# Kernel tuning notes

Hardware: AMD Instinct MI355X
Metric: run time of the kernel (lower is better)

The kernel has to match this reference:

```python
import jax, jax.numpy as jnp
import numpy as np
from jax import lax

B, H, W = 256, 60, 180
NB, NH, OUTC = 37, 128, 64
FILTERS = [1, 64, 128, 128, 64]
FEAT_H, FEAT_W = 4, 12  # spatial dims after 4 SAME 2x2 maxpools
D_LSTM = FEAT_H * OUTC  # 256
LEAK = 0.01
EPS = 1e-5


def setup_inputs() -> dict:
    key = jax.random.key(0)
    ks = jax.random.split(key, 32)
    inp = {"x": jax.random.normal(ks[0], (B, H, W, 1), dtype=jnp.float32)}
    for i in range(4):
        cin, cout = FILTERS[i], FILTERS[i + 1]
        inp[f"w{i}"] = jax.random.normal(ks[1 + i], (3, 3, cin, cout), dtype=jnp.float32) / np.sqrt(9.0 * cin)
        inp[f"cb{i}"] = jnp.zeros((cout,), jnp.float32)
        inp[f"g{i}"] = jnp.ones((cout,), jnp.float32)
        inp[f"bb{i}"] = jnp.zeros((cout,), jnp.float32)
        inp[f"mm{i}"] = 0.1 * jax.random.normal(ks[5 + i], (cout,), dtype=jnp.float32)
        inp[f"mv{i}"] = jax.random.uniform(ks[9 + i], (cout,), minval=0.5, maxval=1.5, dtype=jnp.float32)
    inp["lW0"] = jax.random.normal(ks[13], (D_LSTM + NH, 4 * NH), dtype=jnp.float32) / np.sqrt(D_LSTM + NH)
    inp["lb0"] = jnp.zeros((4 * NH,), jnp.float32)
    inp["lW1"] = jax.random.normal(ks[14], (NH + NH, 4 * NH), dtype=jnp.float32) / np.sqrt(2 * NH)
    inp["lb1"] = jnp.zeros((4 * NH,), jnp.float32)
    inp["Wout"] = jax.random.normal(ks[15], (NH, NB), dtype=jnp.float32) / np.sqrt(NH)
    inp["bout"] = jnp.zeros((NB,), jnp.float32)
    return inp


def _conv_block(x, w, cb, g, bb, mm, mv):
    x = lax.conv_general_dilated(x, w, (1, 1), 'SAME',
                                 dimension_numbers=('NHWC', 'HWIO', 'NHWC')) + cb
    x = (x - mm) * (g * lax.rsqrt(mv + EPS)) + bb          # inference batch norm
    x = jnp.where(x < 0, LEAK * x, x)                       # leaky relu
    x = lax.reduce_window(x, -jnp.inf, lax.max, (1, 2, 2, 1), (1, 2, 2, 1), 'SAME')
    return x


def _lstm_step(c, h, xt, Wk, bk):
    # TF LSTMCell: gates [i, j, f, o], forget_bias=1.0
    z = jnp.concatenate([xt, h], axis=-1) @ Wk + bk
    i, j, f, o = jnp.split(z, 4, axis=-1)
    c = c * jax.nn.sigmoid(f + 1.0) + jax.nn.sigmoid(i) * jnp.tanh(j)
    h = jnp.tanh(c) * jax.nn.sigmoid(o)
    return c, h


def reference(x, w0, cb0, g0, bb0, mm0, mv0, w1, cb1, g1, bb1, mm1, mv1,
              w2, cb2, g2, bb2, mm2, mv2, w3, cb3, g3, bb3, mm3, mv3,
              lW0, lb0, lW1, lb1, Wout, bout):
    for w, cb, g, bb, mm, mv in [(w0, cb0, g0, bb0, mm0, mv0),
                                 (w1, cb1, g1, bb1, mm1, mv1),
                                 (w2, cb2, g2, bb2, mm2, mv2),
                                 (w3, cb3, g3, bb3, mm3, mv3)]:
        x = _conv_block(x, w, cb, g, bb, mm, mv)
    # x: [B, 4, 12, 64] -> [B, T=12, 256]
    x = jnp.transpose(x, (0, 2, 1, 3)).reshape(x.shape[0], FEAT_W, FEAT_H * OUTC)
    xs = jnp.transpose(x, (1, 0, 2))  # [T, B, D]
    b = x.shape[0]
    zeros = jnp.zeros((b, NH), x.dtype)

    def step(carry, xt):
        c0, h0, c1, h1 = carry
        c0, h0 = _lstm_step(c0, h0, xt, lW0, lb0)
        c1, h1 = _lstm_step(c1, h1, h0, lW1, lb1)
        return (c0, h0, c1, h1), h1

    _, hs = lax.scan(step, (zeros, zeros, zeros, zeros), xs)  # [T, B, NH]
    logits = hs @ Wout + bout  # [T, B, nb_classes] (time-major, as in the TF graph)
    return logits
```

## Files before the change

### kernel.cpp

```cpp
#include <hip/hip_runtime.h>
#include <hip/hip_bf16.h>
#include <math.h>
#include <stdint.h>

#define EPS 1e-5f
#define LEAK 0.01f
#define NEG_INF (-3.402823e38f)

typedef __attribute__((ext_vector_type(8))) short short8v;
typedef __attribute__((ext_vector_type(4))) float f32x4;

__device__ __forceinline__ float sigm(float x){ return 1.0f/(1.0f + __expf(-x)); }
__device__ __forceinline__ float tanhf_(float x){ return 1.0f - 2.0f/(__expf(2.0f*x)+1.0f); }
__device__ __forceinline__ float bnl(float a, float sc, float sh){
    float v = fmaf(a, sc, sh);
    return v < 0.0f ? LEAK*v : v;
}
__device__ __forceinline__ unsigned short f2bf(float f){
    __hip_bfloat16 h = __float2bfloat16(f);
    return *reinterpret_cast<unsigned short*>(&h);
}
__device__ __forceinline__ float bf2f(unsigned short u){
    return __uint_as_float(((unsigned)u) << 16);
}

__global__ __launch_bounds__(256) void setup_k(
    const float* __restrict__ w1, const float* __restrict__ w2, const float* __restrict__ w3,
    const float* __restrict__ lW0, const float* __restrict__ lW1, const float* __restrict__ Wout,
    const float* __restrict__ cb0, const float* __restrict__ g0, const float* __restrict__ bb0,
    const float* __restrict__ mm0, const float* __restrict__ mv0,
    const float* __restrict__ cb1, const float* __restrict__ g1, const float* __restrict__ bb1,
    const float* __restrict__ mm1, const float* __restrict__ mv1,
    const float* __restrict__ cb2, const float* __restrict__ g2, const float* __restrict__ bb2,
    const float* __restrict__ mm2, const float* __restrict__ mv2,
    const float* __restrict__ cb3, const float* __restrict__ g3, const float* __restrict__ bb3,
    const float* __restrict__ mm3, const float* __restrict__ mv3,
    unsigned short* __restrict__ Wp1, unsigned short* __restrict__ Wp2, unsigned short* __restrict__ Wp3,
    unsigned short* __restrict__ Wx0p, unsigned short* __restrict__ Wh0p,
    unsigned short* __restrict__ Wx1p, unsigned short* __restrict__ Wh1p,
    unsigned short* __restrict__ WoT, float* __restrict__ bns)
{
    const int bid = blockIdx.x, tid = threadIdx.x;
    if (bid < 864){
        const float* w; unsigned short* wp; int CIN, COUT, base;
        if (bid < 288){ w = w1; wp = Wp1; CIN=64; COUT=128; base = bid; }
        else { w = w2; wp = Wp2; CIN=128; COUT=128; base = bid-288; }
        int t = base*256 + tid;
        int total = 9*CIN*COUT;
        if (t < total){
            int cout = t % COUT, k = t / COUT;
            wp[(size_t)(k>>3)*COUT*8 + (size_t)cout*8 + (k&7)] = f2bf(w[(size_t)k*COUT + cout]);
        }
        return;
    }
    if (bid < 1152){
        int t = (bid-864)*256 + tid;
        if (t < 73728){
            int cout = t % 64, k = t / 64;
            Wp3[(size_t)(k>>3)*64*8 + (size_t)cout*8 + (k&7)] = f2bf(w3[(size_t)k*64 + cout]);
        }
        return;
    }
    if (bid < 2432){
        const float* src; unsigned short* dst; int base;
        if (bid < 1664){ src = lW0; dst = Wx0p; base = bid-1152; }
        else if (bid < 1920){ src = lW0 + 256*512; dst = Wh0p; base = bid-1664; }
        else if (bid < 2176){ src = lW1; dst = Wx1p; base = bid-1920; }
        else { src = lW1 + 128*512; dst = Wh1p; base = bid-2176; }
        int t = base*256 + tid;
        int k = t >> 9, col = t & 511;
        dst[(size_t)(k>>3)*4096 + col*8 + (k&7)] = f2bf(src[(size_t)k*512 + col]);
        return;
    }
    if (bid < 2451){
        int t = (bid-2432)*256 + tid;
        if (t < 4736){
            int n = t >> 7, k = t & 127;
            WoT[t] = f2bf(Wout[k*37 + n]);
        }
        return;
    }
    {
        int t = (bid-2451)*256 + tid;
        if (t < 128){
            float s = g1[t]*rsqrtf(mv1[t]+EPS);
            bns[t] = s; bns[128+t] = fmaf(cb1[t]-mm1[t], s, bb1[t]);
        } else if (t < 256){
            int u = t-128;
            float s = g2[u]*rsqrtf(mv2[u]+EPS);
            bns[256+u] = s; bns[384+u] = fmaf(cb2[u]-mm2[u], s, bb2[u]);
        } else if (t < 320){
            int u = t-256;
            float s = g3[u]*rsqrtf(mv3[u]+EPS);
            bns[512+u] = s; bns[576+u] = fmaf(cb3[u]-mm3[u], s, bb3[u]);
        } else if (t < 384){
            int u = t-320;
            float s = g0[u]*rsqrtf(mv0[u]+EPS);
            bns[640+u] = s; bns[704+u] = fmaf(cb0[u]-mm0[u], s, bb0[u]);
        }
        return;
    }
}

__global__ __launch_bounds__(256) void conv0_k(
    const float* __restrict__ x, const float* __restrict__ w,
    const float* __restrict__ bsc, const float* __restrict__ bsh,
    unsigned short* __restrict__ out, int bbase, int total)
{
    __shared__ float wv[576];
    __shared__ float scs[64], shs[64];
    const int tid = threadIdx.x;
    for (int i=tid;i<576;i+=256) wv[i] = w[i];
    if (tid < 64){ scs[tid]=bsc[tid]; shs[tid]=bsh[tid]; }
    __syncthreads();
    const int id = blockIdx.x*256 + tid;
    if (id >= total) return;
    const int px = id % 90; int r = id / 90; const int py = r % 30; const int b0 = r / 30;
    const float* xb = x + (size_t)(bbase+b0)*10800;
    float p[4][4];
    const int y0 = 2*py-1, xx0 = 2*px-1;
#pragma unroll
    for (int rr=0;rr<4;rr++){
        int yy=y0+rr;
#pragma unroll
        for (int cc=0;cc<4;cc++){
            int xc=xx0+cc;
            p[rr][cc] = (yy>=0&&yy<60&&xc>=0&&xc<180)? xb[yy*180+xc] : 0.f;
        }
    }
    unsigned short* ob = out + (size_t)id*64;
#pragma unroll
    for (int cg=0;cg<8;cg++){
        short8v o8;
#pragma unroll
        for (int j=0;j<8;j++){
            const int co = cg*8+j;
            float s00=0.f,s01=0.f,s10=0.f,s11=0.f;
#pragma unroll
            for (int ky=0;ky<3;ky++)
#pragma unroll
            for (int kx=0;kx<3;kx++){
                float wt = wv[(ky*3+kx)*64+co];
                s00 = fmaf(p[ky][kx],     wt, s00);
                s01 = fmaf(p[ky][kx+1],   wt, s01);
                s10 = fmaf(p[ky+1][kx],   wt, s10);
                s11 = fmaf(p[ky+1][kx+1], wt, s11);
            }
            float sc=scs[co], sh=shs[co];
            float m = fmaxf(fmaxf(bnl(s00,sc,sh),bnl(s01,sc,sh)),
                            fmaxf(bnl(s10,sc,sh),bnl(s11,sc,sh)));
            o8[j] = (short)f2bf(m);
        }
        *(short8v*)&ob[cg*8] = o8;
    }
}

template<int CIN,int COUT,int H,int W>
__global__ __launch_bounds__(256,4) void convmf_k(
    const unsigned short* __restrict__ in, const unsigned short* __restrict__ wp,
    const float* __restrict__ bsc, const float* __restrict__ bsh,
    unsigned short* __restrict__ out)
{
    constexpr int PH=(H+1)/2, PW=(W+1)/2;
    constexpr int HALVES = CIN/64;
    constexpr int NIT = 9*HALVES;
    constexpr int NREP = COUT/16;
    constexpr int CH = (64*COUT)/(256*8);
    __shared__ alignas(16) unsigned short wls[3][64*COUT];

    const int tid = threadIdx.x;
    const int lane = tid & 63;
    const int wm = tid >> 6;
    const int l15 = lane & 15, l4 = lane >> 4;
    const int x0 = blockIdx.x*16, y0 = blockIdx.y*8;
    const int b = blockIdx.z;
    const unsigned short* inb = in + (size_t)b*H*W*CIN;

    int rowoff[4]; bool rowok[4];
#pragma unroll
    for (int j=0;j<4;j++){
        int gy = y0 + 2*wm - 1 + j;
        rowok[j] = (unsigned)gy < (unsigned)H;
        rowoff[j] = (rowok[j] ? gy : 0) * (W*CIN);
    }
    int coloff[3]; bool colok[3];
#pragma unroll
    for (int kx=0;kx<3;kx++){
        int gx = x0 + l15 + kx - 1;
        colok[kx] = (unsigned)gx < (unsigned)W;
        coloff[kx] = (colok[kx] ? gx : 0) * CIN;
    }

    f32x4 acc[2][NREP];
#pragma unroll
    for (int m=0;m<2;m++)
#pragma unroll
    for (int n=0;n<NREP;n++) acc[m][n] = f32x4{0.f,0.f,0.f,0.f};

    auto stageB = [&](int it, int buf){
        const unsigned short* src = wp + (size_t)(it*8)*(COUT*8);
#pragma unroll
        for (int i=0;i<CH;i++){
            const unsigned short* g = src + (size_t)(tid + i*256)*8;
            unsigned short* l = &wls[buf][((tid & ~63) + i*256)*8];
            __builtin_amdgcn_global_load_lds(
                (const __attribute__((address_space(1))) unsigned int*)(uintptr_t)g,
                (__attribute__((address_space(3))) unsigned int*)(uintptr_t)l,
                16, 0, 0);
        }
    };

    stageB(0, 0);
    if (NIT > 1) stageB(1, 1);
    if constexpr (CH == 4){ asm volatile("s_waitcnt vmcnt(4)" ::: "memory"); }
    else                  { asm volatile("s_waitcnt vmcnt(2)" ::: "memory"); }
    __builtin_amdgcn_sched_barrier(0);
    __builtin_amdgcn_s_barrier();

    for (int it=0; it<NIT; ++it){
        const int tap = it / HALVES;
        const int khalf = it - tap*HALVES;
        const int ky = tap/3, kx = tap - ky*3;
        const int cin0 = khalf*64 + l4*8;
        const short8v z8 = short8v{0,0,0,0,0,0,0,0};
        short8v a[2][2];
#pragma unroll
        for (int rf=0;rf<2;rf++){
            const int j = rf + ky;
            const bool ok = rowok[j] && colok[kx];
            const unsigned short* p = inb + rowoff[j] + coloff[kx] + cin0;
#pragma unroll
            for (int ks=0;ks<2;ks++){
                short8v v = *(const short8v*)(p + ks*32);
                a[rf][ks] = ok ? v : z8;
            }
        }
        __builtin_amdgcn_sched_barrier(0);
        if (it+2 < NIT) stageB(it+2, (it+2)%3);
        __builtin_amdgcn_sched_barrier(0);
        const unsigned short* wb = &wls[it%3][0];
        __builtin_amdgcn_s_setprio(1);
#pragma unroll
        for (int ks=0; ks<2; ++ks){
#pragma unroll
            for (int nf=0; nf<NREP; ++nf){
                short8v bfr = *(const short8v*)&wb[((ks*4+l4)*COUT + nf*16 + l15)*8];
                acc[0][nf] = __builtin_amdgcn_mfma_f32_16x16x32_bf16(a[0][ks], bfr, acc[0][nf],0,0,0);
                acc[1][nf] = __builtin_amdgcn_mfma_f32_16x16x32_bf16(a[1][ks], bfr, acc[1][nf],0,0,0);
            }
        }
        __builtin_amdgcn_s_setprio(0);
        __builtin_amdgcn_s_barrier();
    }

    const int pr = (y0>>1) + wm;
    if (pr < PH){
        const bool r1 = (y0 + 2*wm + 1) < H;
        unsigned short* ob = out + ((size_t)b*PH + pr)*PW*COUT;
#pragma unroll
        for (int nf=0; nf<NREP; ++nf){
            const int co = nf*16 + l15;
            const float scv = bsc[co], shv = bsh[co];
            f32x4 e = acc[0][nf], o = acc[1][nf];
#pragma unroll
            for (int pp=0; pp<2; ++pp){
                const int pc = (x0>>1) + l4*2 + pp;
                if (pc >= PW) continue;
                const int oddcol = x0 + l4*4 + 2*pp + 1;
                float m = bnl(e[2*pp], scv, shv);
                if (oddcol < W) m = fmaxf(m, bnl(e[2*pp+1], scv, shv));
                if (r1){
                    m = fmaxf(m, bnl(o[2*pp], scv, shv));
                    if (oddcol < W) m = fmaxf(m, bnl(o[2*pp+1], scv, shv));
                }
                ob[(size_t)pc*COUT + co] = f2bf(m);
            }
        }
    }
}

template<int K, int MODE>
__global__ __launch_bounds__(256) void gemmrow_k(
    const unsigned short* __restrict__ A, const unsigned short* __restrict__ wp,
    const float* __restrict__ bias, float* __restrict__ out)
{
    constexpr int NS = K/32;
    __shared__ alignas(16) unsigned short wls[2][16384];
    const int tid = threadIdx.x, lane = tid & 63, w = tid >> 6;
    const int l15 = lane & 15, l4 = lane >> 4;
    const int r0 = blockIdx.x*32;

    f32x4 acc[2][8];
#pragma unroll
    for (int m=0;m<2;m++)
#pragma unroll
    for (int n=0;n<8;n++) acc[m][n] = f32x4{0.f,0.f,0.f,0.f};

    auto stage = [&](int s, int buf){
        const unsigned short* src = wp + (size_t)s*16384;
#pragma unroll
        for (int i=0;i<8;i++){
            int e = (tid + i*256)*8;
            *(short8v*)&wls[buf][e] = *(const short8v*)&src[e];
        }
    };
    stage(0,0);
    __syncthreads();

    for (int s=0;s<NS;++s){
        const int k0 = s*32 + l4*8;
        short8v af[2];
#pragma unroll
        for (int mf=0;mf<2;++mf){
            const int row = r0 + mf*16 + l15;
            size_t idx;
            if constexpr (MODE == 0){
                const int b = row & 255, t = row >> 8;
                idx = (size_t)b*3072 + (k0>>6)*768 + t*64 + (k0&63);
            } else {
                idx = (size_t)row*K + k0;
            }
            af[mf] = *(const short8v*)&A[idx];
        }
        if (s+1 < NS) stage(s+1,(s+1)&1);
        const unsigned short* wb = &wls[s&1][0];
#pragma unroll
        for (int nf=0;nf<8;++nf){
            const int col = w*128 + nf*16 + l15;
            short8v bfr = *(const short8v*)&wb[(l4*512 + col)*8];
#pragma unroll
            for (int mf=0;mf<2;++mf)
                acc[mf][nf] = __builtin_amdgcn_mfma_f32_16x16x32_bf16(af[mf], bfr, acc[mf][nf], 0,0,0);
        }
        __syncthreads();
    }
#pragma unroll
    for (int nf=0;nf<8;++nf){
        const int col = w*128 + nf*16 + l15;
        const float bv = bias[col];
#pragma unroll
        for (int mf=0;mf<2;++mf){
#pragma unroll
            for (int j=0;j<4;++j){
                const int row = r0 + mf*16 + l4*4 + j;
                out[(size_t)row*512 + col] = acc[mf][nf][j] + bv;
            }
        }
    }
}

__global__ __launch_bounds__(512) void lstm0_k(
    const float* __restrict__ xp, const unsigned short* __restrict__ wh0p,
    unsigned short* __restrict__ h0g)
{
    __shared__ alignas(16) unsigned short wl[65536];
    __shared__ alignas(16) float hb[128];
    __shared__ float zs[512];
    const int col = threadIdx.x;
    const int b = blockIdx.x;
#pragma unroll
    for (int i=0;i<16;i++){
        int e = (col + i*512)*8;
        *(short8v*)&wl[e] = *(const short8v*)&wh0p[e];
    }
    if (col < 128) hb[col] = 0.f;
    float c0 = 0.f;
    __syncthreads();

    for (int t=0;t<12;t++){
        float acc = xp[((size_t)t*256 + b)*512 + col];
#pragma unroll 4
        for (int kg=0;kg<16;kg++){
            short8v w8 = *(const short8v*)&wl[(kg*512 + col)*8];
            float4 hlo = *(const float4*)&hb[kg*8];
            float4 hhi = *(const float4*)&hb[kg*8+4];
            acc = fmaf(bf2f((unsigned short)w8[0]), hlo.x, acc);
            acc = fmaf(bf2f((unsigned short)w8[1]), hlo.y, acc);
            acc = fmaf(bf2f((unsigned short)w8[2]), hlo.z, acc);
            acc = fmaf(bf2f((unsigned short)w8[3]), hlo.w, acc);
            acc = fmaf(bf2f((unsigned short)w8[4]), hhi.x, acc);
            acc = fmaf(bf2f((unsigned short)w8[5]), hhi.y, acc);
            acc = fmaf(bf2f((unsigned short)w8[6]), hhi.z, acc);
            acc = fmaf(bf2f((unsigned short)w8[7]), hhi.w, acc);
        }
        zs[col] = acc;
        __syncthreads();
        if (col < 128){
            float zi=zs[col], zj=zs[128+col], zf=zs[256+col], zo=zs[384+col];
            c0 = c0*sigm(zf+1.f) + sigm(zi)*tanhf_(zj);
            float h = tanhf_(c0)*sigm(zo);
            hb[col] = h;
            h0g[((size_t)t*256 + b)*128 + col] = f2bf(h);
        }
        __syncthreads();
    }
}

__global__ __launch_bounds__(512) void lstm1_k(
    const float* __restrict__ zp1, const unsigned short* __restrict__ wh1p,
    const unsigned short* __restrict__ woT, const float* __restrict__ bout,
    float* __restrict__ out)
{
    __shared__ alignas(16) unsigned short wl[65536];
    __shared__ alignas(16) float hb[128];
    __shared__ float zs[512];
    __shared__ float red[37][8];
    const int col = threadIdx.x;
    const int b = blockIdx.x;
#pragma unroll
    for (int i=0;i<16;i++){
        int e = (col + i*512)*8;
        *(short8v*)&wl[e] = *(const short8v*)&wh1p[e];
    }
    if (col < 128) hb[col] = 0.f;
    float c1 = 0.f;
    __syncthreads();

    for (int t=0;t<12;t++){
        float acc = zp1[((size_t)t*256 + b)*512 + col];
#pragma unroll 4
        for (int kg=0;kg<16;kg++){
            short8v w8 = *(const short8v*)&wl[(kg*512 + col)*8];
            float4 hlo = *(const float4*)&hb[kg*8];
            float4 hhi = *(const float4*)&hb[kg*8+4];
            acc = fmaf(bf2f((unsigned short)w8[0]), hlo.x, acc);
            acc = fmaf(bf2f((unsigned short)w8[1]), hlo.y, acc);
            acc = fmaf(bf2f((unsigned short)w8[2]), hlo.z, acc);
            acc = fmaf(bf2f((unsigned short)w8[3]), hlo.w, acc);
            acc = fmaf(bf2f((unsigned short)w8[4]), hhi.x, acc);
            acc = fmaf(bf2f((unsigned short)w8[5]), hhi.y, acc);
            acc = fmaf(bf2f((unsigned short)w8[6]), hhi.z, acc);
            acc = fmaf(bf2f((unsigned short)w8[7]), hhi.w, acc);
        }
        zs[col] = acc;
        __syncthreads();
        if (col < 128){
            float zi=zs[col], zj=zs[128+col], zf=zs[256+col], zo=zs[384+col];
            c1 = c1*sigm(zf+1.f) + sigm(zi)*tanhf_(zj);
            hb[col] = tanhf_(c1)*sigm(zo);
        }
        __syncthreads();
        if (col < 296){
            const int n = col >> 3, q = col & 7;
            float p0 = 0.f;
#pragma unroll
            for (int kk=0;kk<16;kk++){
                float wv2 = bf2f(woT[n*128 + q*16 + kk]);
                p0 = fmaf(hb[q*16+kk], wv2, p0);
            }
            red[n][q] = p0;
        }
        __syncthreads();
        if (col < 37){
            float s0 = bout[col];
#pragma unroll
            for (int q=0;q<8;q++) s0 += red[col][q];
            out[((size_t)t*256 + b)*37 + col] = s0;
        }
        __syncthreads();
    }
}

extern "C" void kernel_launch(void* const* d_in, const int* in_sizes, int n_in,
                              void* d_out, int out_size, void* d_ws, size_t ws_size,
                              hipStream_t stream) {
    const float* x = (const float*)d_in[0];
    const float *w_[4], *cb_[4], *g_[4], *bb_[4], *mm_[4], *mv_[4];
    for (int i=0;i<4;i++){
        w_[i]  = (const float*)d_in[1+6*i];
        cb_[i] = (const float*)d_in[2+6*i];
        g_[i]  = (const float*)d_in[3+6*i];
        bb_[i] = (const float*)d_in[4+6*i];
        mm_[i] = (const float*)d_in[5+6*i];
        mv_[i] = (const float*)d_in[6+6*i];
    }
    const float* lW0  = (const float*)d_in[25];
    const float* lb0  = (const float*)d_in[26];
    const float* lW1  = (const float*)d_in[27];
    const float* lb1  = (const float*)d_in[28];
    const float* Wout = (const float*)d_in[29];
    const float* bout = (const float*)d_in[30];
    float* out = (float*)d_out;

    const size_t fixed = 6291456ull + 6291456 + 4096 + 1572864 + 786432
                       + 147456 + 294912 + 147456
                       + 262144 + 131072 + 131072 + 131072 + 9472;
    int Bc = 256;
    while (Bc > 8 && fixed + (size_t)Bc*565504 > ws_size) Bc >>= 1;

    char* cur = (char*)d_ws;
    float* XP  = (float*)cur;                    cur += 6291456;
    float* ZP1 = (float*)cur;                    cur += 6291456;
    float* bns = (float*)cur;                    cur += 4096;
    unsigned short* F    = (unsigned short*)cur; cur += 1572864;
    unsigned short* h0g  = (unsigned short*)cur; cur += 786432;
    unsigned short* Wp1  = (unsigned short*)cur; cur += 147456;
    unsigned short* Wp2  = (unsigned short*)cur; cur += 294912;
    unsigned short* Wp3  = (unsigned short*)cur; cur += 147456;
    unsigned short* Wx0p = (unsigned short*)cur; cur += 262144;
    unsigned short* Wh0p = (unsigned short*)cur; cur += 131072;
    unsigned short* Wx1p = (unsigned short*)cur; cur += 131072;
    unsigned short* Wh1p = (unsigned short*)cur; cur += 131072;
    unsigned short* WoT  = (unsigned short*)cur; cur += 9472;
    unsigned short* A    = (unsigned short*)cur; cur += (size_t)Bc*345600;
    unsigned short* Bb   = (unsigned short*)cur; cur += (size_t)Bc*172800;
    unsigned short* C    = (unsigned short*)cur;

    setup_k<<<2453, 256, 0, stream>>>(
        w_[1], w_[2], w_[3], lW0, lW1, Wout,
        cb_[0],g_[0],bb_[0],mm_[0],mv_[0],
        cb_[1],g_[1],bb_[1],mm_[1],mv_[1],
        cb_[2],g_[2],bb_[2],mm_[2],mv_[2],
        cb_[3],g_[3],bb_[3],mm_[3],mv_[3],
        Wp1, Wp2, Wp3, Wx0p, Wh0p, Wx1p, Wh1p, WoT, bns);

    const int nc = 256 / Bc;
    for (int bc=0; bc<nc; bc++){
        int bbase = bc*Bc;
        conv0_k<<<(Bc*2700+255)/256, 256, 0, stream>>>(x, w_[0], bns+640, bns+704, A, bbase, Bc*2700);
        convmf_k<64,128,30,90><<<dim3(6,4,Bc), 256, 0, stream>>>(A, Wp1, bns+0, bns+128, Bb);
        convmf_k<128,128,15,45><<<dim3(3,2,Bc), 256, 0, stream>>>(Bb, Wp2, bns+256, bns+384, C);
        convmf_k<128,64,8,23><<<dim3(2,1,Bc), 256, 0, stream>>>(C, Wp3, bns+512, bns+576,
                                                                F + (size_t)bbase*3072);
    }
    gemmrow_k<256,0><<<96, 256, 0, stream>>>(F, Wx0p, lb0, XP);
    lstm0_k<<<256, 512, 0, stream>>>(XP, Wh0p, h0g);
    gemmrow_k<128,1><<<96, 256, 0, stream>>>(h0g, Wx1p, lb1, ZP1);
    lstm1_k<<<256, 512, 0, stream>>>(ZP1, Wh1p, WoT, bout, out);
}
```

Measured before the change: 397.8 us.

## Stage conv input halo tile in LDS with swizzle; double-buffer weights

The MFMA conv kernel now loads a 10x18 input halo tile (all input channels) into shared memory once, with an XOR swizzle against bank conflicts. The A fragments for every tap then come from LDS instead of repeated global loads. The weight ring buffer drops from three stages to two, prefetching one step ahead with __syncthreads. Occupancy launch bounds drop from 4 to 2 blocks per CU because the LDS footprint is much larger (up to ~46KB for CIN=128). The risks are lower occupancy, a serialized prologue load, and less weight-prefetch depth.

```diff
diff --git a/kernel.cpp b/kernel.cpp
--- a/kernel.cpp
+++ b/kernel.cpp
@@ -156,7 +156,7 @@
 }
 
 template<int CIN,int COUT,int H,int W>
-__global__ __launch_bounds__(256,4) void convmf_k(
+__global__ __launch_bounds__(256,2) void convmf_k(
     const unsigned short* __restrict__ in, const unsigned short* __restrict__ wp,
     const float* __restrict__ bsc, const float* __restrict__ bsh,
     unsigned short* __restrict__ out)
@@ -166,7 +166,10 @@
     constexpr int NIT = 9*HALVES;
     constexpr int NREP = COUT/16;
     constexpr int CH = (64*COUT)/(256*8);
-    __shared__ alignas(16) unsigned short wls[3][64*COUT];
+    constexpr int AR = 10, AC = 18;
+    constexpr int AV = AR*AC*(CIN/8);
+    __shared__ alignas(16) unsigned short als[AR*AC*CIN];
+    __shared__ alignas(16) unsigned short wls[2][64*COUT];
 
     const int tid = threadIdx.x;
     const int lane = tid & 63;
@@ -176,21 +179,6 @@
     const int b = blockIdx.z;
     const unsigned short* inb = in + (size_t)b*H*W*CIN;
 
-    int rowoff[4]; bool rowok[4];
-#pragma unroll
-    for (int j=0;j<4;j++){
-        int gy = y0 + 2*wm - 1 + j;
-        rowok[j] = (unsigned)gy < (unsigned)H;
-        rowoff[j] = (rowok[j] ? gy : 0) * (W*CIN);
-    }
-    int coloff[3]; bool colok[3];
-#pragma unroll
-    for (int kx=0;kx<3;kx++){
-        int gx = x0 + l15 + kx - 1;
-        colok[kx] = (unsigned)gx < (unsigned)W;
-        coloff[kx] = (colok[kx] ? gx : 0) * CIN;
-    }
-
     f32x4 acc[2][NREP];
 #pragma unroll
     for (int m=0;m<2;m++)
@@ -211,34 +199,39 @@
     };
 
     stageB(0, 0);
-    if (NIT > 1) stageB(1, 1);
-    if constexpr (CH == 4){ asm volatile("s_waitcnt vmcnt(4)" ::: "memory"); }
-    else                  { asm volatile("s_waitcnt vmcnt(2)" ::: "memory"); }
-    __builtin_amdgcn_sched_barrier(0);
-    __builtin_amdgcn_s_barrier();
+    {
+        const short8v z8 = short8v{0,0,0,0,0,0,0,0};
+        for (int v = tid; v < AV; v += 256){
+            const int cin8 = v % (CIN/8);
+            const int rc = v / (CIN/8);
+            const int col = rc % AC, row = rc / AC;
+            const int gy = y0 - 1 + row, gx = x0 - 1 + col;
+            short8v val = z8;
+            if ((unsigned)gy < (unsigned)H && (unsigned)gx < (unsigned)W)
+                val = *(const short8v*)&inb[((size_t)gy*W + gx)*CIN + cin8*8];
+            int elem = ((row*AC + col)*CIN + cin8*8) ^ ((col & 7) << 3);
+            *(short8v*)&als[elem] = val;
+        }
+    }
+    __syncthreads();
 
     for (int it=0; it<NIT; ++it){
+        if (it+1 < NIT) stageB(it+1, (it+1)&1);
         const int tap = it / HALVES;
         const int khalf = it - tap*HALVES;
         const int ky = tap/3, kx = tap - ky*3;
-        const int cin0 = khalf*64 + l4*8;
-        const short8v z8 = short8v{0,0,0,0,0,0,0,0};
         short8v a[2][2];
 #pragma unroll
         for (int rf=0;rf<2;rf++){
-            const int j = rf + ky;
-            const bool ok = rowok[j] && colok[kx];
-            const unsigned short* p = inb + rowoff[j] + coloff[kx] + cin0;
-#pragma unroll
-            for (int ks=0;ks<2;ks++){
-                short8v v = *(const short8v*)(p + ks*32);
-                a[rf][ks] = ok ? v : z8;
-            }
-        }
-        __builtin_amdgcn_sched_barrier(0);
-        if (it+2 < NIT) stageB(it+2, (it+2)%3);
-        __builtin_amdgcn_sched_barrier(0);
-        const unsigned short* wb = &wls[it%3][0];
+            const int lrow = 2*wm + rf + ky;
+            const int col_l = l15 + kx;
+            const int base = (lrow*AC + col_l)*CIN + khalf*64 + l4*8;
+            const int swz = (col_l & 7) << 3;
+#pragma unroll
+            for (int ks=0;ks<2;ks++)
+                a[rf][ks] = *(const short8v*)&als[(base + ks*32) ^ swz];
+        }
+        const unsigned short* wb = &wls[it&1][0];
         __builtin_amdgcn_s_setprio(1);
 #pragma unroll
         for (int ks=0; ks<2; ++ks){
@@ -250,7 +243,7 @@
             }
         }
         __builtin_amdgcn_s_setprio(0);
-        __builtin_amdgcn_s_barrier();
+        __syncthreads();
     }
 
     const int pr = (y0>>1) + wm;
```

Measured after the change: 373.3 us. -6.2%, faster.
